# Kernel tuning notes

Measured on AMD Instinct MI355X. Metric: run time of the kernel, lower is better.

## Reference

```python
import jax, jax.numpy as jnp
import numpy as np

KSIZE = 13
DIL = 3
NUM_HEADS = 4
LN_EPS = 1e-5


def _na_idx(L, k, d):
    # NATTEN-style dilated neighborhood indices along one axis.
    i = jnp.arange(L)
    g, ii = i % d, i // d                       # dilation group, index within group
    Lg = (L - g + d - 1) // d                   # group length per position
    start = jnp.clip(ii - k // 2, 0, Lg - k)    # clamped window start (group coords)
    offs = jnp.arange(k)
    nbr = g[:, None] + d * (start[:, None] + offs[None, :])           # (L,k) absolute idx
    rel = start[:, None] + offs[None, :] - ii[:, None] + (k - 1)      # (L,k) rpb index in [0,2k-2]
    return nbr, rel


def _layernorm(x, g, b):
    mu = jnp.mean(x, -1, keepdims=True)
    var = jnp.mean(jnp.square(x - mu), -1, keepdims=True)
    return (x - mu) * jax.lax.rsqrt(var + LN_EPS) * g + b


def setup_inputs() -> dict:
    key = jax.random.key(0)
    ks = jax.random.split(key, 12)
    B, H, W, C = 1, 96, 96, 64
    mh = int(C * 4.0)
    s = 0.02
    return {
        "x": jax.random.normal(ks[0], (B, H * W, C), jnp.float32),
        "norm1_g": jnp.ones((C,), jnp.float32),
        "norm1_b": jnp.zeros((C,), jnp.float32),
        "qkv_w": jax.random.normal(ks[1], (C, 3 * C), jnp.float32) * s,
        "qkv_b": jnp.zeros((3 * C,), jnp.float32),
        "rpb": jax.random.normal(ks[2], (NUM_HEADS, 2 * KSIZE - 1, 2 * KSIZE - 1), jnp.float32) * s,
        "proj_w": jax.random.normal(ks[3], (C, C), jnp.float32) * s,
        "proj_b": jnp.zeros((C,), jnp.float32),
        "norm2_g": jnp.ones((C,), jnp.float32),
        "norm2_b": jnp.zeros((C,), jnp.float32),
        "fc1_w": jax.random.normal(ks[4], (C, mh), jnp.float32) * s,
        "fc1_b": jnp.zeros((mh,), jnp.float32),
        "fc2_w": jax.random.normal(ks[5], (mh, C), jnp.float32) * s,
        "fc2_b": jnp.zeros((C,), jnp.float32),
        "H": H,
        "W": W,
    }


def _ga(h, qkv_w, qkv_b, rpb, proj_w, proj_b):
    # h: (B,H,W,C) -> dilated neighborhood attention, kernel=13, dilation=3
    B, H, W, C = h.shape
    nh, hd = NUM_HEADS, C // NUM_HEADS
    scale = hd ** -0.5
    qkv = (h @ qkv_w + qkv_b).reshape(B, H, W, 3, nh, hd)
    qkv = qkv.transpose(3, 0, 4, 1, 2, 5)       # (3,B,nh,H,W,hd)
    q, k, v = qkv[0] * scale, qkv[1], qkv[2]
    idx_h, rel_h = _na_idx(H, KSIZE, DIL)
    idx_w, rel_w = _na_idx(W, KSIZE, DIL)
    Kk = KSIZE

    def gather(t):  # (B,nh,H,W,hd) -> (B,nh,H,W,Kk*Kk,hd)
        t = jnp.take(t, idx_h, axis=2)          # (B,nh,H,Kk,W,hd)
        t = jnp.take(t, idx_w, axis=4)          # (B,nh,H,Kk,W,Kk,hd)
        return t.transpose(0, 1, 2, 4, 3, 5, 6).reshape(B, nh, H, W, Kk * Kk, hd)

    kg = gather(k)
    vg = gather(v)
    logits = jnp.einsum('bnhwc,bnhwkc->bnhwk', q, kg)
    bias = rpb[:, rel_h]                         # (nh,H,Kk,2K-1)
    bias = bias[:, :, :, rel_w]                  # (nh,H,Kk,W,Kk)
    bias = bias.transpose(0, 1, 3, 2, 4).reshape(nh, H, W, Kk * Kk)
    attn = jax.nn.softmax(logits + bias[None], axis=-1)
    out = jnp.einsum('bnhwk,bnhwkc->bnhwc', attn, vg)
    out = out.transpose(0, 2, 3, 1, 4).reshape(B, H, W, C)
    return out @ proj_w + proj_b


def reference(x, norm1_g, norm1_b, qkv_w, qkv_b, rpb, proj_w, proj_b,
              norm2_g, norm2_b, fc1_w, fc1_b, fc2_w, fc2_b, H, W):
    B, N, C = x.shape
    shortcut = x
    h = _layernorm(x, norm1_g, norm1_b).reshape(B, H, W, C)
    h = _ga(h, qkv_w, qkv_b, rpb, proj_w, proj_b).reshape(B, N, C)
    x = shortcut + h
    h2 = _layernorm(x, norm2_g, norm2_b)
    mlp = jax.nn.gelu(h2 @ fc1_w + fc1_b, approximate=False) @ fc2_w + fc2_b
    return x + mlp
```

## Files before the change

kernel.cpp:

```cpp
#include <hip/hip_runtime.h>
#include <math.h>

#define HH 96
#define WW 96
#define CC 64
#define NH 4
#define HD 16
#define KS 13
#define KK (KS*KS)
#define NTOK (HH*WW)

template<int CTRL>
__device__ __forceinline__ float dpp_add(float p) {
    int t = __builtin_amdgcn_update_dpp(0, __float_as_int(p), CTRL, 0xF, 0xF, true);
    return p + __int_as_float(t);
}

__device__ __forceinline__ float dpp_reduce8(float p) {
    p = dpp_add<0xB1>(p);
    p = dpp_add<0x4E>(p);
    p = dpp_add<0x141>(p);
    return p;
}

__device__ __forceinline__ void ln_rows32(float (*buf)[34],
                                          const float* __restrict__ g,
                                          const float* __restrict__ b,
                                          int tid) {
    int r  = tid >> 3;
    int c0 = (tid & 7) * 8;
    float v[8];
    float s = 0.0f;
    #pragma unroll
    for (int j = 0; j < 8; j++) { v[j] = buf[c0 + j][r]; s += v[j]; }
    s = dpp_reduce8(s);
    float mu = s * (1.0f / 64.0f);
    float s2 = 0.0f;
    #pragma unroll
    for (int j = 0; j < 8; j++) { float d = v[j] - mu; s2 += d * d; }
    s2 = dpp_reduce8(s2);
    float inv = rsqrtf(s2 * (1.0f / 64.0f) + 1e-5f);
    #pragma unroll
    for (int j = 0; j < 8; j++)
        buf[c0 + j][r] = (v[j] - mu) * inv * g[c0 + j] + b[c0 + j];
}

__global__ __launch_bounds__(256) void ln_gemm_kernel(const float* __restrict__ x,
                                                      const float* __restrict__ g,
                                                      const float* __restrict__ b,
                                                      const float* __restrict__ W,
                                                      const float* __restrict__ bias,
                                                      float* __restrict__ out) {
    __shared__ float Ast[64][34];
    const int t0 = blockIdx.x * 32;
    const int tid = threadIdx.x;

    for (int i = tid; i < 32 * 64; i += 256) {
        int r = i >> 6, cc = i & 63;
        Ast[cc][r] = x[t0 * 64 + i];
    }
    __syncthreads();
    ln_rows32(Ast, g, b, tid);
    __syncthreads();

    const int tc = tid & 15;
    const int tr = tid >> 4;
    const int r0 = tr * 2;
    const int c  = blockIdx.y * 64 + tc * 4;

    float4 b4 = *(const float4*)&bias[c];
    float4 acc0 = b4, acc1 = b4;
    #pragma unroll 8
    for (int k = 0; k < 64; k++) {
        float2 a = *(const float2*)&Ast[k][r0];
        float4 w = *(const float4*)&W[k * 192 + c];
        acc0.x += a.x * w.x; acc0.y += a.x * w.y; acc0.z += a.x * w.z; acc0.w += a.x * w.w;
        acc1.x += a.y * w.x; acc1.y += a.y * w.y; acc1.z += a.y * w.z; acc1.w += a.y * w.w;
    }
    if (blockIdx.y == 0) {
        acc0.x *= 0.25f; acc0.y *= 0.25f; acc0.z *= 0.25f; acc0.w *= 0.25f;
        acc1.x *= 0.25f; acc1.y *= 0.25f; acc1.z *= 0.25f; acc1.w *= 0.25f;
    }
    *(float4*)&out[(t0 + r0) * 192 + c] = acc0;
    *(float4*)&out[(t0 + r0 + 1) * 192 + c] = acc1;
}

__global__ __launch_bounds__(256) void na_attn_kernel(const float* __restrict__ qkv,
                                                      const float* __restrict__ rpb,
                                                      float* __restrict__ out) {
    int wave = threadIdx.x >> 6;
    int lane = threadIdx.x & 63;
    int token = blockIdx.x * 4 + wave;
    int head = lane >> 4;
    int slot = (lane >> 2) & 3;
    int l    = lane & 3;
    int co   = head * HD + l * 4;

    int y = token / WW, x = token - y * WW;
    int gh = y % 3, ih = y / 3;
    int gw = x % 3, iw = x / 3;
    int sh = ih - 6; sh = sh < 0 ? 0 : (sh > 19 ? 19 : sh);
    int sw = iw - 6; sw = sw < 0 ? 0 : (sw > 19 ? 19 : sw);

    float4 q4 = *(const float4*)&qkv[token * 192 + co];
    const float* bias_h = rpb + head * 625 + (sw - iw + 12);

    const int xpart = (gw + 3 * sw) * 192 + 64 + co + slot * 576;

    float4 acc = make_float4(0.f, 0.f, 0.f, 0.f);
    float s = 0.0f;

    for (int kh = 0; kh < KS; kh++) {
        int ny = gh + 3 * (sh + kh);
        const float* kp = qkv + ny * (WW * 192) + xpart;
        const float* bp = bias_h + (sh + kh - ih + 12) * 25;
        #pragma unroll
        for (int i = 0; i < 3; i++) {
            float4 k4 = *(const float4*)(kp + i * 2304);
            float4 v4 = *(const float4*)(kp + i * 2304 + 64);
            float p = q4.x * k4.x + q4.y * k4.y + q4.z * k4.z + q4.w * k4.w;
            p = dpp_add<0xB1>(p);
            p = dpp_add<0x4E>(p);
            float e = __expf(p + bp[4 * i + slot]);
            s += e;
            acc.x += e * v4.x; acc.y += e * v4.y; acc.z += e * v4.z; acc.w += e * v4.w;
        }
        if (slot == 0) {
            float4 k4 = *(const float4*)(kp + 3 * 2304);
            float4 v4 = *(const float4*)(kp + 3 * 2304 + 64);
            float p = q4.x * k4.x + q4.y * k4.y + q4.z * k4.z + q4.w * k4.w;
            p = dpp_add<0xB1>(p);
            p = dpp_add<0x4E>(p);
            float e = __expf(p + bp[12]);
            s += e;
            acc.x += e * v4.x; acc.y += e * v4.y; acc.z += e * v4.z; acc.w += e * v4.w;
        }
    }

    s = dpp_add<0x128>(s);  s = dpp_add<0x124>(s);
    acc.x = dpp_add<0x128>(acc.x); acc.x = dpp_add<0x124>(acc.x);
    acc.y = dpp_add<0x128>(acc.y); acc.y = dpp_add<0x124>(acc.y);
    acc.z = dpp_add<0x128>(acc.z); acc.z = dpp_add<0x124>(acc.z);
    acc.w = dpp_add<0x128>(acc.w); acc.w = dpp_add<0x124>(acc.w);

    if (slot == 0) {
        float inv = 1.0f / s;
        *(float4*)&out[token * CC + co] =
            make_float4(acc.x * inv, acc.y * inv, acc.z * inv, acc.w * inv);
    }
}

__global__ __launch_bounds__(256) void mlp_fused_kernel(const float* __restrict__ attn_out,
                                                        const float* __restrict__ x,
                                                        const float* __restrict__ proj_w,
                                                        const float* __restrict__ proj_b,
                                                        const float* __restrict__ n2g,
                                                        const float* __restrict__ n2b,
                                                        const float* __restrict__ fc1_w,
                                                        const float* __restrict__ fc1_b,
                                                        const float* __restrict__ fc2_w,
                                                        const float* __restrict__ fc2_b,
                                                        float* __restrict__ out) {
    __shared__ float Ast[64][34];
    __shared__ float X2T[64][34];
    __shared__ float Hid[256][34];

    const int t0 = blockIdx.x * 32;
    const int tid = threadIdx.x;

    for (int i = tid; i < 32 * 64; i += 256) {
        int r = i >> 6, cc = i & 63;
        Ast[cc][r] = attn_out[t0 * 64 + i];
    }
    __syncthreads();

    const int tc = tid & 15;
    const int tr = tid >> 4;
    const int r0 = tr * 2;
    const int c  = tc * 4;

    float4 pb = *(const float4*)&proj_b[c];
    float4 a0 = pb, a1 = pb;
    #pragma unroll 8
    for (int k = 0; k < 64; k++) {
        float2 a = *(const float2*)&Ast[k][r0];
        float4 w = *(const float4*)&proj_w[k * 64 + c];
        a0.x += a.x * w.x; a0.y += a.x * w.y; a0.z += a.x * w.z; a0.w += a.x * w.w;
        a1.x += a.y * w.x; a1.y += a.y * w.y; a1.z += a.y * w.z; a1.w += a.y * w.w;
    }
    {
        float4 x0 = *(const float4*)&x[(t0 + r0) * 64 + c];
        float4 x1 = *(const float4*)&x[(t0 + r0 + 1) * 64 + c];
        a0.x += x0.x; a0.y += x0.y; a0.z += x0.z; a0.w += x0.w;
        a1.x += x1.x; a1.y += x1.y; a1.z += x1.z; a1.w += x1.w;
    }
    X2T[c + 0][r0] = a0.x; X2T[c + 1][r0] = a0.y; X2T[c + 2][r0] = a0.z; X2T[c + 3][r0] = a0.w;
    X2T[c + 0][r0 + 1] = a1.x; X2T[c + 1][r0 + 1] = a1.y; X2T[c + 2][r0 + 1] = a1.z; X2T[c + 3][r0 + 1] = a1.w;
    __syncthreads();

    ln_rows32(X2T, n2g, n2b, tid);
    __syncthreads();

    float4 h0[4], h1[4];
    #pragma unroll
    for (int gg = 0; gg < 4; gg++) {
        float4 bb = *(const float4*)&fc1_b[c + gg * 64];
        h0[gg] = bb; h1[gg] = bb;
    }
    #pragma unroll 4
    for (int k = 0; k < 64; k++) {
        float2 a = *(const float2*)&X2T[k][r0];
        #pragma unroll
        for (int gg = 0; gg < 4; gg++) {
            float4 w = *(const float4*)&fc1_w[k * 256 + c + gg * 64];
            h0[gg].x += a.x * w.x; h0[gg].y += a.x * w.y; h0[gg].z += a.x * w.z; h0[gg].w += a.x * w.w;
            h1[gg].x += a.y * w.x; h1[gg].y += a.y * w.y; h1[gg].z += a.y * w.z; h1[gg].w += a.y * w.w;
        }
    }
    #define GELU1(v) v = 0.5f * v * (1.0f + erff(v * 0.70710678118f))
    #pragma unroll
    for (int gg = 0; gg < 4; gg++) {
        GELU1(h0[gg].x); GELU1(h0[gg].y); GELU1(h0[gg].z); GELU1(h0[gg].w);
        GELU1(h1[gg].x); GELU1(h1[gg].y); GELU1(h1[gg].z); GELU1(h1[gg].w);
    }
    #undef GELU1
    #pragma unroll
    for (int gg = 0; gg < 4; gg++) {
        int col = c + gg * 64;
        Hid[col + 0][r0] = h0[gg].x; Hid[col + 1][r0] = h0[gg].y;
        Hid[col + 2][r0] = h0[gg].z; Hid[col + 3][r0] = h0[gg].w;
        Hid[col + 0][r0 + 1] = h1[gg].x; Hid[col + 1][r0 + 1] = h1[gg].y;
        Hid[col + 2][r0 + 1] = h1[gg].z; Hid[col + 3][r0 + 1] = h1[gg].w;
    }
    __syncthreads();

    float4 ob = *(const float4*)&fc2_b[c];
    float4 o0 = ob, o1 = ob;
    #pragma unroll 8
    for (int k = 0; k < 256; k++) {
        float2 a = *(const float2*)&Hid[k][r0];
        float4 w = *(const float4*)&fc2_w[k * 64 + c];
        o0.x += a.x * w.x; o0.y += a.x * w.y; o0.z += a.x * w.z; o0.w += a.x * w.w;
        o1.x += a.y * w.x; o1.y += a.y * w.y; o1.z += a.y * w.z; o1.w += a.y * w.w;
    }
    o0.x += a0.x; o0.y += a0.y; o0.z += a0.z; o0.w += a0.w;
    o1.x += a1.x; o1.y += a1.y; o1.z += a1.z; o1.w += a1.w;
    *(float4*)&out[(t0 + r0) * 64 + c] = o0;
    *(float4*)&out[(t0 + r0 + 1) * 64 + c] = o1;
}

extern "C" void kernel_launch(void* const* d_in, const int* in_sizes, int n_in,
                              void* d_out, int out_size, void* d_ws, size_t ws_size,
                              hipStream_t stream) {
    const float* x       = (const float*)d_in[0];
    const float* norm1_g = (const float*)d_in[1];
    const float* norm1_b = (const float*)d_in[2];
    const float* qkv_w   = (const float*)d_in[3];
    const float* qkv_b   = (const float*)d_in[4];
    const float* rpb     = (const float*)d_in[5];
    const float* proj_w  = (const float*)d_in[6];
    const float* proj_b  = (const float*)d_in[7];
    const float* norm2_g = (const float*)d_in[8];
    const float* norm2_b = (const float*)d_in[9];
    const float* fc1_w   = (const float*)d_in[10];
    const float* fc1_b   = (const float*)d_in[11];
    const float* fc2_w   = (const float*)d_in[12];
    const float* fc2_b   = (const float*)d_in[13];
    float* out = (float*)d_out;

    float* ws = (float*)d_ws;
    float* qkv      = ws;
    float* attn_out = qkv + NTOK * 192;

    dim3 blk(256);
    ln_gemm_kernel<<<dim3(NTOK / 32, 3), blk, 0, stream>>>(x, norm1_g, norm1_b, qkv_w, qkv_b, qkv);
    na_attn_kernel<<<NTOK / 4, blk, 0, stream>>>(qkv, rpb, attn_out);
    mlp_fused_kernel<<<NTOK / 32, blk, 0, stream>>>(attn_out, x, proj_w, proj_b,
                                                    norm2_g, norm2_b, fc1_w, fc1_b,
                                                    fc2_w, fc2_b, out);
}
```

Baseline: 171.7 us.

## Process four same-group query tokens per wave with shared column window

Remaps the attention kernel so each wave handles four neighboring queries in one dilation group, and each lane iterates over a shared 16-column window with masking. This replaces splitting one token's 13 columns across four slots. The intent is to share K/V loads across queries and drop the cross-slot reduction. In exchange, each lane does more exp and FMA work, including masked columns, and the grid has fewer blocks.

```diff
diff --git a/kernel.cpp b/kernel.cpp
--- a/kernel.cpp
+++ b/kernel.cpp
@@ -90,64 +90,58 @@
                                                       float* __restrict__ out) {
     int wave = threadIdx.x >> 6;
     int lane = threadIdx.x & 63;
-    int token = blockIdx.x * 4 + wave;
+    int wid  = blockIdx.x * 4 + wave;
+    int y    = wid / 24;
+    int rem  = wid - y * 24;
+    int g    = rem >> 3;
+    int iw0  = (rem & 7) * 4;
+
     int head = lane >> 4;
-    int slot = (lane >> 2) & 3;
+    int u    = (lane >> 2) & 3;
     int l    = lane & 3;
     int co   = head * HD + l * 4;
 
-    int y = token / WW, x = token - y * WW;
+    int iwu   = iw0 + u;
+    int token = y * WW + g + 3 * iwu;
+
     int gh = y % 3, ih = y / 3;
-    int gw = x % 3, iw = x / 3;
     int sh = ih - 6; sh = sh < 0 ? 0 : (sh > 19 ? 19 : sh);
-    int sw = iw - 6; sw = sw < 0 ? 0 : (sw > 19 ? 19 : sw);
+    int swu = iwu - 6; swu = swu < 0 ? 0 : (swu > 19 ? 19 : swu);
+    int cbase = iw0 - 6; cbase = cbase < 0 ? 0 : (cbase > 19 ? 19 : cbase);
 
     float4 q4 = *(const float4*)&qkv[token * 192 + co];
-    const float* bias_h = rpb + head * 625 + (sw - iw + 12);
-
-    const int xpart = (gw + 3 * sw) * 192 + 64 + co + slot * 576;
+    const float* bias_h = rpb + head * 625;
 
     float4 acc = make_float4(0.f, 0.f, 0.f, 0.f);
     float s = 0.0f;
 
     for (int kh = 0; kh < KS; kh++) {
         int ny = gh + 3 * (sh + kh);
-        const float* kp = qkv + ny * (WW * 192) + xpart;
-        const float* bp = bias_h + (sh + kh - ih + 12) * 25;
+        int rh = sh + kh - ih + 12;
+        const float* rowp = qkv + (ny * WW + g) * 192 + 64 + co;
+        const float* brow = bias_h + rh * 25;
         #pragma unroll
-        for (int i = 0; i < 3; i++) {
-            float4 k4 = *(const float4*)(kp + i * 2304);
-            float4 v4 = *(const float4*)(kp + i * 2304 + 64);
+        for (int j = 0; j < 16; j++) {
+            int c  = cbase + j;
+            int cl = c > 31 ? 31 : c;
+            float4 k4 = *(const float4*)(rowp + cl * 576);
+            float4 v4 = *(const float4*)(rowp + cl * 576 + 64);
+            int rel = c - iwu + 12;
+            float bias = brow[rel > 24 ? 24 : rel];
+            unsigned kw = (unsigned)(c - swu);
+            bias = (kw <= 12u) ? bias : -1e30f;
             float p = q4.x * k4.x + q4.y * k4.y + q4.z * k4.z + q4.w * k4.w;
             p = dpp_add<0xB1>(p);
             p = dpp_add<0x4E>(p);
-            float e = __expf(p + bp[4 * i + slot]);
+            float e = __expf(p + bias);
             s += e;
             acc.x += e * v4.x; acc.y += e * v4.y; acc.z += e * v4.z; acc.w += e * v4.w;
         }
-        if (slot == 0) {
-            float4 k4 = *(const float4*)(kp + 3 * 2304);
-            float4 v4 = *(const float4*)(kp + 3 * 2304 + 64);
-            float p = q4.x * k4.x + q4.y * k4.y + q4.z * k4.z + q4.w * k4.w;
-            p = dpp_add<0xB1>(p);
-            p = dpp_add<0x4E>(p);
-            float e = __expf(p + bp[12]);
-            s += e;
-            acc.x += e * v4.x; acc.y += e * v4.y; acc.z += e * v4.z; acc.w += e * v4.w;
-        }
-    }
-
-    s = dpp_add<0x128>(s);  s = dpp_add<0x124>(s);
-    acc.x = dpp_add<0x128>(acc.x); acc.x = dpp_add<0x124>(acc.x);
-    acc.y = dpp_add<0x128>(acc.y); acc.y = dpp_add<0x124>(acc.y);
-    acc.z = dpp_add<0x128>(acc.z); acc.z = dpp_add<0x124>(acc.z);
-    acc.w = dpp_add<0x128>(acc.w); acc.w = dpp_add<0x124>(acc.w);
-
-    if (slot == 0) {
-        float inv = 1.0f / s;
-        *(float4*)&out[token * CC + co] =
-            make_float4(acc.x * inv, acc.y * inv, acc.z * inv, acc.w * inv);
-    }
+    }
+
+    float inv = 1.0f / s;
+    *(float4*)&out[token * CC + co] =
+        make_float4(acc.x * inv, acc.y * inv, acc.z * inv, acc.w * inv);
 }
 
 __global__ __launch_bounds__(256) void mlp_fused_kernel(const float* __restrict__ attn_out,
@@ -274,7 +268,7 @@
 
     dim3 blk(256);
     ln_gemm_kernel<<<dim3(NTOK / 32, 3), blk, 0, stream>>>(x, norm1_g, norm1_b, qkv_w, qkv_b, qkv);
-    na_attn_kernel<<<NTOK / 4, blk, 0, stream>>>(qkv, rpb, attn_out);
+    na_attn_kernel<<<NTOK / 16, blk, 0, stream>>>(qkv, rpb, attn_out);
     mlp_fused_kernel<<<NTOK / 32, blk, 0, stream>>>(attn_out, x, proj_w, proj_b,
                                                     norm2_g, norm2_b, fc1_w, fc1_b,
                                                     fc2_w, fc2_b, out);
```

Measured after the change: 205.2 us. +19.5%, slower.
